# Kernel optimization log

Measured on AMD Instinct MI355X. Metric: run time of the kernel, lower is better.

Reference implementation:

```python
import jax, jax.numpy as jnp
import numpy as np

K_CHUNK = 512  # key-chunk size used by the module when n > 5000


def setup_inputs() -> dict:
    key = jax.random.key(0)
    ks = jax.random.split(key, 9)
    b, n, d = 1, 8192, 512
    s = 1.0 / np.sqrt(d)
    x = jax.random.normal(ks[0], (b, n, d), dtype=jnp.float32)
    Wq = jax.random.normal(ks[1], (d, d), dtype=jnp.float32) * s
    bq = jax.random.normal(ks[2], (d,), dtype=jnp.float32) * 0.01
    Wk = jax.random.normal(ks[3], (d, d), dtype=jnp.float32) * s
    bk = jax.random.normal(ks[4], (d,), dtype=jnp.float32) * 0.01
    Wv = jax.random.normal(ks[5], (d, d), dtype=jnp.float32) * s
    bv = jax.random.normal(ks[6], (d,), dtype=jnp.float32) * 0.01
    Wo = jax.random.normal(ks[7], (d, d), dtype=jnp.float32) * s
    bo = jax.random.normal(ks[8], (d,), dtype=jnp.float32) * 0.01
    return {"x": x, "Wq": Wq, "bq": bq, "Wk": Wk, "bk": bk,
            "Wv": Wv, "bv": bv, "Wo": Wo, "bo": bo}


def reference(x, Wq, bq, Wk, bk, Wv, bv, Wo, bo):
    # Faithful to the n > 5000 branch of SimpleAttenLayer (eval mode: dropout = identity).
    # The q-chunking in the original does not change the math (each q row is independent),
    # so we vectorize over all queries. The k-chunking DOES change the math: softmax is
    # applied within each 512-wide key block, then a second softmax over the concatenated
    # per-block weights, then matmul with full v.
    b, n, d = x.shape
    assert n % K_CHUNK == 0
    q = x @ Wq + bq
    k = x @ Wk + bk
    v = x @ Wv + bv
    scores = jnp.einsum('bnd,bmd->bnm', q, k) / jnp.sqrt(jnp.float32(d))
    # softmax within each key chunk of size K_CHUNK
    w1 = jax.nn.softmax(scores.reshape(b, n, n // K_CHUNK, K_CHUNK), axis=-1)
    w1 = w1.reshape(b, n, n)
    # second (global) softmax over the concatenated chunk weights
    w2 = jax.nn.softmax(w1, axis=-1)
    attn_out = jnp.einsum('bnm,bmd->bnd', w2, v)
    cls_attn_weights = w2[:, 0:1, :]  # [b, 1, n]
    out = x + (attn_out @ Wo + bo)
    return (out, cls_attn_weights)
```

## Files before the change

### kernel.cpp

```cpp
#include <hip/hip_runtime.h>
#include <stdint.h>

typedef unsigned short u16;
typedef uint8_t u8;
typedef __bf16 bf16x8 __attribute__((ext_vector_type(8)));
typedef float f32x4 __attribute__((ext_vector_type(4)));

#define NTOK 8192
#define DD 512
#define CHK 512
#define NCH 16
#define KSPLIT 4
#define KLEN 2048
#define LOG2E 1.4426950408889634f
#define SCL 0.044194173824159216f
#define SCLL 0.063762069130835270f

__device__ __forceinline__ u16 f2bf(float f) {
  union { float f; uint32_t u; } v; v.f = f;
  uint32_t r = v.u + 0x7FFFu + ((v.u >> 16) & 1u);
  return (u16)(r >> 16);
}

template <int CTRL>
__device__ __forceinline__ float dppadd(float x) {
  int y = __builtin_amdgcn_update_dpp(0, __float_as_int(x), CTRL, 0xF, 0xF, true);
  return x + __int_as_float(y);
}
__device__ __forceinline__ float rowsum16(float x) {
  x = dppadd<0xB1>(x);
  x = dppadd<0x4E>(x);
  x = dppadd<0x141>(x);
  x = dppadd<0x140>(x);
  return x;
}

typedef const __attribute__((address_space(1))) unsigned int* gas_t;
typedef __attribute__((address_space(3))) unsigned int* las_t;
__device__ __forceinline__ void gload16(const void* g, void* l) {
  __builtin_amdgcn_global_load_lds((gas_t)g, (las_t)l, 16, 0, 0);
}

__device__ __forceinline__ int permtok(int t) {
  return (t & ~63) | (((t & 15) << 2) | ((t >> 4) & 3));
}

__global__ void prep_kernel(const float* __restrict__ x, const float* __restrict__ Wq,
                            const float* __restrict__ Wk, const float* __restrict__ Wv,
                            const float* __restrict__ Wo, const float* __restrict__ bq,
                            u16* __restrict__ xb, u16* __restrict__ Wall, u16* __restrict__ WoT,
                            float* __restrict__ lsum, float* __restrict__ q0g) {
  __shared__ float t[32][33];
  const int bid = blockIdx.x;
  const int tid = threadIdx.x;
  if (bid < 4096) {
    int i = bid * 256 + tid;
    if (bid < 32) lsum[bid * 256 + tid] = 0.f;
    float4 v = ((const float4*)x)[i];
    ushort4 o;
    o.x = f2bf(v.x); o.y = f2bf(v.y); o.z = f2bf(v.z); o.w = f2bf(v.w);
    ((ushort4*)xb)[i] = o;
  } else if (bid < 5120) {
    const int tt = bid - 4096;
    const int z = tt >> 8, idx = tt & 255;
    const float* W; u16* WT;
    if (z == 0)      { W = Wq; WT = Wall; }
    else if (z == 1) { W = Wk; WT = Wall + 512 * 512; }
    else if (z == 2) { W = Wv; WT = Wall + 2 * 512 * 512; }
    else             { W = Wo; WT = WoT; }
    const int n0 = (idx & 15) * 32, k0 = (idx >> 4) * 32;
    const int tx = tid & 31, ty = tid >> 5;
    #pragma unroll
    for (int i = 0; i < 4; i++)
      t[ty + 8 * i][tx] = W[(k0 + ty + 8 * i) * DD + n0 + tx];
    __syncthreads();
    #pragma unroll
    for (int i = 0; i < 4; i++)
      WT[(n0 + ty + 8 * i) * DD + k0 + tx] = f2bf(t[tx][ty + 8 * i]);
  } else {
    const int c = (bid - 5120) * 256 + tid;
    float acc = bq[c];
    #pragma unroll 8
    for (int i = 0; i < 512; i++) acc += x[i] * Wq[i * 512 + c];
    q0g[c] = acc;
  }
}

__launch_bounds__(256, 3)
__global__ void qkv_kernel(const u16* __restrict__ A, const u16* __restrict__ Wall,
                           const float* __restrict__ bq, const float* __restrict__ bk,
                           const float* __restrict__ bv, u8* __restrict__ qb8,
                           u8* __restrict__ kb8, u8* __restrict__ vT8) {
  __shared__ __align__(16) u16 As[128 * 32];
  __shared__ __align__(16) u16 Bs[128 * 32];
  const int m0 = blockIdx.x * 128;
  const int n0g = blockIdx.y * 128;
  const int which = blockIdx.y >> 2;
  const int n0 = n0g & 511;
  const int tid = threadIdx.x;
  const int w = tid >> 6, lane = tid & 63, lm = lane & 15, quad = lane >> 4;
  const int wm = w & 1, wn = w >> 1;
  f32x4 acc[4][4] = {};
  const int soff = tid * 16;
  const int srow = soff >> 6;
  const int scol = soff & 63;
  const char* Ag = (const char*)A + ((size_t)(m0 + srow) * DD) * 2 + scol;
  const char* Bg = (const char*)Wall + ((size_t)(n0g + srow) * DD) * 2 + scol;
  char* Al = (char*)As + w * 1024;
  char* Bl = (char*)Bs + w * 1024;
  const size_t rs = (size_t)64 * DD * 2;
  for (int kk = 0; kk < DD; kk += 32) {
    const char* ag = Ag + (size_t)kk * 2;
    const char* bg = Bg + (size_t)kk * 2;
    gload16(ag, Al);
    gload16(ag + rs, Al + 4096);
    gload16(bg, Bl);
    gload16(bg + rs, Bl + 4096);
    __syncthreads();
    bf16x8 af[4], bfr[4];
    #pragma unroll
    for (int i = 0; i < 4; i++) af[i] = *(const bf16x8*)&As[(wm * 64 + i * 16 + lm) * 32 + quad * 8];
    #pragma unroll
    for (int j = 0; j < 4; j++) bfr[j] = *(const bf16x8*)&Bs[(wn * 64 + j * 16 + lm) * 32 + quad * 8];
    #pragma unroll
    for (int i = 0; i < 4; i++)
      #pragma unroll
      for (int j = 0; j < 4; j++)
        acc[i][j] = __builtin_amdgcn_mfma_f32_16x16x32_bf16(af[i], bfr[j], acc[i][j], 0, 0, 0);
    __syncthreads();
  }
  const float* bias = (which == 0) ? bq : (which == 1) ? bk : bv;
  #pragma unroll
  for (int i = 0; i < 4; i++) {
    const int row0 = m0 + wm * 64 + i * 16 + quad * 4;
    #pragma unroll
    for (int j = 0; j < 4; j++) {
      const int col = n0 + wn * 64 + j * 16 + lm;
      const float bv_ = bias[col];
      if (which == 2) {
        #pragma unroll
        for (int r = 0; r < 4; r++) {
          const float val = acc[i][j][r] + bv_;
          uint32_t pk = __builtin_amdgcn_cvt_pk_fp8_f32(val, val, 0, false);
          vT8[(size_t)col * NTOK + permtok(row0 + r)] = (u8)(pk & 0xFF);
        }
      } else {
        u8* dst = (which == 0) ? qb8 : kb8;
        #pragma unroll
        for (int r = 0; r < 4; r++) {
          const float val = acc[i][j][r] + bv_;
          uint32_t pk = __builtin_amdgcn_cvt_pk_fp8_f32(val, val, 0, false);
          dst[(size_t)(row0 + r) * DD + col] = (u8)(pk & 0xFF);
        }
      }
    }
  }
}

__launch_bounds__(256, 3)
__global__ void outproj_kernel(const u16* __restrict__ A, const u16* __restrict__ BT,
                               const float* __restrict__ bias, float* __restrict__ outp,
                               const float* __restrict__ resid) {
  __shared__ __align__(16) u16 As[128 * 32];
  __shared__ __align__(16) u16 Bs[128 * 32];
  const int m0 = blockIdx.x * 128, n0 = blockIdx.y * 128;
  const int tid = threadIdx.x;
  const int w = tid >> 6, lane = tid & 63, lm = lane & 15, quad = lane >> 4;
  const int wm = w & 1, wn = w >> 1;
  f32x4 acc[4][4] = {};
  const int soff = tid * 16;
  const int srow = soff >> 6;
  const int scol = soff & 63;
  const char* Ag = (const char*)A + ((size_t)(m0 + srow) * DD) * 2 + scol;
  const char* Bg = (const char*)BT + ((size_t)(n0 + srow) * DD) * 2 + scol;
  char* Al = (char*)As + w * 1024;
  char* Bl = (char*)Bs + w * 1024;
  const size_t rs = (size_t)64 * DD * 2;
  for (int kk = 0; kk < DD; kk += 32) {
    const char* ag = Ag + (size_t)kk * 2;
    const char* bg = Bg + (size_t)kk * 2;
    gload16(ag, Al);
    gload16(ag + rs, Al + 4096);
    gload16(bg, Bl);
    gload16(bg + rs, Bl + 4096);
    __syncthreads();
    bf16x8 af[4], bfr[4];
    #pragma unroll
    for (int i = 0; i < 4; i++) af[i] = *(const bf16x8*)&As[(wm * 64 + i * 16 + lm) * 32 + quad * 8];
    #pragma unroll
    for (int j = 0; j < 4; j++) bfr[j] = *(const bf16x8*)&Bs[(wn * 64 + j * 16 + lm) * 32 + quad * 8];
    #pragma unroll
    for (int i = 0; i < 4; i++)
      #pragma unroll
      for (int j = 0; j < 4; j++)
        acc[i][j] = __builtin_amdgcn_mfma_f32_16x16x32_bf16(af[i], bfr[j], acc[i][j], 0, 0, 0);
    __syncthreads();
  }
  #pragma unroll
  for (int i = 0; i < 4; i++) {
    const int row0 = m0 + wm * 64 + i * 16 + quad * 4;
    #pragma unroll
    for (int j = 0; j < 4; j++) {
      const int col = n0 + wn * 64 + j * 16 + lm;
      const float bv = bias[col];
      #pragma unroll
      for (int r = 0; r < 4; r++) {
        const size_t idx = (size_t)(row0 + r) * DD + col;
        outp[idx] = acc[i][j][r] + bv + resid[idx];
      }
    }
  }
}

template <int MODE>
__launch_bounds__(256, 3)
__global__ void gemm_fp8_kernel(const u8* __restrict__ A, const u8* __restrict__ BT,
                                int K, int lda, int ldb, void* __restrict__ outp,
                                const float* __restrict__ lsum) {
  __shared__ __align__(16) u8 As[128 * 64];
  __shared__ __align__(16) u8 Bs[128 * 64];
  const int m0 = blockIdx.x * 128, n0 = blockIdx.y * 128;
  const int tid = threadIdx.x;
  const int w = tid >> 6, lane = tid & 63, lm = lane & 15, quad = lane >> 4;
  const int wm = w & 1, wn = w >> 1;
  f32x4 acc[4][4] = {};
  const int srow = tid >> 2;
  const int scol = ((tid & 3) ^ ((srow >> 1) & 3)) * 16;
  const size_t kbase = (MODE == 4) ? (size_t)blockIdx.z * (size_t)K : 0;
  const u8* Ag = A + (size_t)(m0 + srow) * lda + kbase + scol;
  const u8* Bg = BT + (size_t)(n0 + srow) * ldb + kbase + scol;
  u8* Al = As + w * 1024;
  u8* Bl = Bs + w * 1024;
  const size_t ars = (size_t)64 * lda;
  const size_t brs = (size_t)64 * ldb;
  const int swz = (lm >> 1) & 3;
  const int off8 = (quad & 1) * 8;
  const int cg0 = quad >> 1;
  for (int kk = 0; kk < K; kk += 64) {
    const u8* ag = Ag + kk;
    const u8* bg = Bg + kk;
    gload16(ag, Al);
    gload16(ag + ars, Al + 4096);
    gload16(bg, Bl);
    gload16(bg + brs, Bl + 4096);
    __syncthreads();
    #pragma unroll
    for (int kk2 = 0; kk2 < 64; kk2 += 32) {
      const int csel = ((cg0 + (kk2 >> 4)) ^ swz) * 16 + off8;
      long af[4], bfr[4];
      #pragma unroll
      for (int i = 0; i < 4; i++)
        af[i] = *(const long*)&As[(wm * 64 + i * 16 + lm) * 64 + csel];
      #pragma unroll
      for (int j = 0; j < 4; j++)
        bfr[j] = *(const long*)&Bs[(wn * 64 + j * 16 + lm) * 64 + csel];
      #pragma unroll
      for (int i = 0; i < 4; i++)
        #pragma unroll
        for (int j = 0; j < 4; j++)
          acc[i][j] = __builtin_amdgcn_mfma_f32_16x16x32_fp8_fp8(af[i], bfr[j], acc[i][j], 0, 0, 0);
    }
    __syncthreads();
  }
  #pragma unroll
  for (int i = 0; i < 4; i++) {
    const int row0 = m0 + wm * 64 + i * 16 + quad * 4;
    float li[4];
    if (MODE == 3) {
      #pragma unroll
      for (int r = 0; r < 4; r++) li[r] = 1.0f / lsum[row0 + r];
    }
    #pragma unroll
    for (int j = 0; j < 4; j++) {
      const int col = n0 + wn * 64 + j * 16 + lm;
      if (MODE == 3) {
        #pragma unroll
        for (int r = 0; r < 4; r++)
          ((u16*)outp)[(size_t)(row0 + r) * DD + col] = f2bf(acc[i][j][r] * li[r]);
      } else {
        float* po = (float*)outp + (size_t)blockIdx.z * NTOK * DD;
        #pragma unroll
        for (int r = 0; r < 4; r++)
          po[(size_t)(row0 + r) * DD + col] = acc[i][j][r];
      }
    }
  }
}

__global__ void pv_reduce_kernel(const float* __restrict__ part, const float* __restrict__ lsum,
                                 u16* __restrict__ attnb) {
  const int idx = blockIdx.x * 256 + threadIdx.x;
  const int row = idx >> 7;
  const int c4 = (idx & 127) << 2;
  const float* p = part + (size_t)row * DD + c4;
  const size_t stride = (size_t)NTOK * DD;
  float4 a = *(const float4*)(p);
  float4 b = *(const float4*)(p + stride);
  float4 c = *(const float4*)(p + 2 * stride);
  float4 d = *(const float4*)(p + 3 * stride);
  const float inv = 1.0f / lsum[row];
  ushort4 o;
  o.x = f2bf((a.x + b.x + c.x + d.x) * inv);
  o.y = f2bf((a.y + b.y + c.y + d.y) * inv);
  o.z = f2bf((a.z + b.z + c.z + d.z) * inv);
  o.w = f2bf((a.w + b.w + c.w + d.w) * inv);
  *(ushort4*)(attnb + (size_t)row * DD + c4) = o;
}

__launch_bounds__(1024, 4)
__global__ void scores_kernel(const u8* __restrict__ qb8, const u8* __restrict__ kb8,
                              u8* __restrict__ P8, float* __restrict__ lsum) {
  __shared__ __align__(16) u8 As[128 * 64];
  __shared__ __align__(16) u8 Bs[512 * 64];
  __shared__ float hS[8][128], hP[8][128], hZ[128];
  const int m0 = blockIdx.x * 128;
  const int c = blockIdx.y;
  const int tid = threadIdx.x;
  const int w = tid >> 6, lane = tid & 63, lm = lane & 15, quad = lane >> 4;
  const int mt = w & 1, wsl = w >> 1;
  f32x4 s[4][4] = {};
  const int srA = tid >> 2;
  const int scS = ((tid & 3) ^ ((srA >> 1) & 3)) * 16;
  const u8* Qg = qb8 + (size_t)(m0 + srA) * DD + scS;
  const u8* Kg = kb8 + (size_t)(c * CHK + srA) * DD + scS;
  u8* Al = As + w * 1024;
  u8* Bl = Bs + w * 1024;
  const int swz = (lm >> 1) & 3;
  const int off8 = (quad & 1) * 8;
  const int cg0 = quad >> 1;
  for (int kk = 0; kk < DD; kk += 64) {
    if (tid < 512) gload16(Qg + kk, Al);
    gload16(Kg + kk, Bl);
    gload16(Kg + kk + (size_t)256 * DD, Bl + 16384);
    __syncthreads();
    #pragma unroll
    for (int kk2 = 0; kk2 < 64; kk2 += 32) {
      const int csel = ((cg0 + (kk2 >> 4)) ^ swz) * 16 + off8;
      long af[4], bfr[4];
      #pragma unroll
      for (int i = 0; i < 4; i++)
        af[i] = *(const long*)&As[(mt * 64 + i * 16 + lm) * 64 + csel];
      #pragma unroll
      for (int j = 0; j < 4; j++)
        bfr[j] = *(const long*)&Bs[(wsl * 64 + j * 16 + lm) * 64 + csel];
      #pragma unroll
      for (int i = 0; i < 4; i++)
        #pragma unroll
        for (int j = 0; j < 4; j++)
          s[i][j] = __builtin_amdgcn_mfma_f32_16x16x32_fp8_fp8(af[i], bfr[j], s[i][j], 0, 0, 0);
    }
    __syncthreads();
  }
  #pragma unroll
  for (int i = 0; i < 4; i++) {
    #pragma unroll
    for (int reg = 0; reg < 4; reg++) {
      float z = 0.f;
      #pragma unroll
      for (int j = 0; j < 4; j++) {
        float e = exp2f(s[i][j][reg] * SCLL);
        s[i][j][reg] = e;
        z += e;
      }
      z = rowsum16(z);
      if (lm == 0) hS[wsl][mt * 64 + i * 16 + quad * 4 + reg] = z;
    }
  }
  __syncthreads();
  if (tid < 128) {
    float t = 0.f;
    #pragma unroll
    for (int w2 = 0; w2 < 8; w2++) t += hS[w2][tid];
    hZ[tid] = LOG2E / t;
  }
  __syncthreads();
  #pragma unroll
  for (int i = 0; i < 4; i++) {
    #pragma unroll
    for (int reg = 0; reg < 4; reg++) {
      const int rl = mt * 64 + i * 16 + quad * 4 + reg;
      const float iz = hZ[rl];
      const float p0 = exp2f(s[i][0][reg] * iz);
      const float p1 = exp2f(s[i][1][reg] * iz);
      const float p2 = exp2f(s[i][2][reg] * iz);
      const float p3 = exp2f(s[i][3][reg] * iz);
      float zp = (p0 + p1) + (p2 + p3);
      zp = rowsum16(zp);
      if (lm == 0) hP[wsl][rl] = zp;
      uint32_t o = __builtin_amdgcn_cvt_pk_fp8_f32(p0, p1, 0, false);
      o = __builtin_amdgcn_cvt_pk_fp8_f32(p2, p3, o, true);
      *(uint32_t*)(P8 + (size_t)(m0 + rl) * NTOK + c * CHK + wsl * 64 + lm * 4) = o;
    }
  }
  __syncthreads();
  if (tid < 128) {
    float t = 0.f;
    #pragma unroll
    for (int w2 = 0; w2 < 8; w2++) t += hP[w2][tid];
    atomicAdd(&lsum[m0 + tid], t);
  }
}

__global__ void cls_u_kernel(const float* __restrict__ Wk, const float* __restrict__ bk,
                             const float* __restrict__ q0g, float* __restrict__ uc) {
  __shared__ float q0[512];
  const int tid = threadIdx.x;
  q0[tid] = q0g[tid];
  q0[tid + 256] = q0g[tid + 256];
  __syncthreads();
  if (blockIdx.x < 8) {
    const int c = blockIdx.x * 64 + (tid >> 2), ii = tid & 3;
    float acc = 0.f;
    #pragma unroll 8
    for (int j = ii; j < 512; j += 4) acc += Wk[(size_t)c * 512 + j] * q0[j];
    acc += __shfl_xor(acc, 1, 64);
    acc += __shfl_xor(acc, 2, 64);
    if (ii == 0) uc[c] = acc;
  } else if (tid < 64) {
    float acc = 0.f;
    #pragma unroll 8
    for (int j = tid; j < 512; j += 64) acc += bk[j] * q0[j];
    #pragma unroll
    for (int off = 1; off < 64; off <<= 1) acc += __shfl_xor(acc, off, 64);
    if (tid == 0) uc[512] = acc;
  }
}

__global__ void cls_scores_kernel(const float* __restrict__ x, const float* __restrict__ uc,
                                  float* __restrict__ s0) {
  __shared__ float u[512];
  __shared__ float c0s;
  int tid = threadIdx.x;
  for (int i = tid; i < 512; i += 256) u[i] = uc[i];
  if (tid == 0) c0s = uc[512];
  __syncthreads();
  int rowg = blockIdx.x * 32 + (tid >> 3);
  int ii = tid & 7;
  const float* xr = x + rowg * 512;
  float acc = 0.f;
  for (int i = ii; i < 512; i += 8) acc += xr[i] * u[i];
  acc += __shfl_xor(acc, 1, 64);
  acc += __shfl_xor(acc, 2, 64);
  acc += __shfl_xor(acc, 4, 64);
  if (ii == 0) s0[rowg] = (acc + c0s) * SCL;
}

__global__ void cls_softmax_kernel(const float* __restrict__ s0, float* __restrict__ out) {
  int tid = threadIdx.x;
  int w = tid >> 6, lane = tid & 63;
  const float* sc = s0 + w * 512;
  float v[8];
  float m = -1e30f;
  #pragma unroll
  for (int j = 0; j < 8; j++) { v[j] = sc[lane * 8 + j]; m = fmaxf(m, v[j]); }
  for (int off = 1; off < 64; off <<= 1) m = fmaxf(m, __shfl_xor(m, off, 64));
  float z = 0.f;
  #pragma unroll
  for (int j = 0; j < 8; j++) { v[j] = expf(v[j] - m); z += v[j]; }
  for (int off = 1; off < 64; off <<= 1) z += __shfl_xor(z, off, 64);
  float invz = 1.f / z;
  float l = 0.f;
  #pragma unroll
  for (int j = 0; j < 8; j++) { v[j] = expf(v[j] * invz); l += v[j]; }
  for (int off = 1; off < 64; off <<= 1) l += __shfl_xor(l, off, 64);
  __shared__ float lw[16];
  if (lane == 0) lw[w] = l;
  __syncthreads();
  float L = 0.f;
  for (int i = 0; i < 16; i++) L += lw[i];
  float invL = 1.f / L;
  #pragma unroll
  for (int j = 0; j < 8; j++) out[w * 512 + lane * 8 + j] = v[j] * invL;
}

extern "C" void kernel_launch(void* const* d_in, const int* in_sizes, int n_in,
                              void* d_out, int out_size, void* d_ws, size_t ws_size,
                              hipStream_t stream) {
  const float* x  = (const float*)d_in[0];
  const float* Wq = (const float*)d_in[1];
  const float* bq = (const float*)d_in[2];
  const float* Wk = (const float*)d_in[3];
  const float* bk = (const float*)d_in[4];
  const float* Wv = (const float*)d_in[5];
  const float* bv = (const float*)d_in[6];
  const float* Wo = (const float*)d_in[7];
  const float* bo = (const float*)d_in[8];
  float* out = (float*)d_out;

  char* ws = (char*)d_ws;
  u16* xb    = (u16*)(ws);
  u16* Wall  = (u16*)(ws + 8388608);
  u16* WoT   = (u16*)(ws + 9961472);
  u8*  qb8   = (u8*)(ws + 10485760);
  u8*  kb8   = (u8*)(ws + 14680064);
  u8*  vT8   = (u8*)(ws + 18874368);
  u16* attnb = (u16*)(ws + 23068672);
  float* q0g = (float*)(ws + 31457280);
  float* uc  = (float*)(ws + 31461376);
  float* s0  = (float*)(ws + 31465472);
  float* lsum= (float*)(ws + 31498240);
  u8*  P8    = (u8*)(ws + 31531008);
  float* part= (float*)(ws + 98639872);
  const size_t need_full = 98639872ULL + (size_t)KSPLIT * NTOK * DD * 4ULL;

  prep_kernel<<<5122, 256, 0, stream>>>(x, Wq, Wk, Wv, Wo, bq, xb, Wall, WoT, lsum, q0g);

  qkv_kernel<<<dim3(NTOK / 128, 12), 256, 0, stream>>>(xb, Wall, bq, bk, bv, qb8, kb8, vT8);

  scores_kernel<<<dim3(NTOK / 128, NCH), 1024, 0, stream>>>(qb8, kb8, P8, lsum);

  if (ws_size >= need_full) {
    gemm_fp8_kernel<4><<<dim3(NTOK / 128, DD / 128, KSPLIT), 256, 0, stream>>>(
        P8, vT8, KLEN, NTOK, NTOK, part, nullptr);
    pv_reduce_kernel<<<NTOK * DD / 4 / 256, 256, 0, stream>>>(part, lsum, attnb);
  } else {
    gemm_fp8_kernel<3><<<dim3(NTOK / 128, DD / 128), 256, 0, stream>>>(
        P8, vT8, NTOK, NTOK, NTOK, attnb, lsum);
  }

  outproj_kernel<<<dim3(NTOK / 128, DD / 128), 256, 0, stream>>>(attnb, WoT, bo, out, x);

  cls_u_kernel<<<9, 256, 0, stream>>>(Wk, bk, q0g, uc);
  cls_scores_kernel<<<NTOK / 32, 256, 0, stream>>>(x, uc, s0);
  cls_softmax_kernel<<<1, 1024, 0, stream>>>(s0, out + (size_t)NTOK * DD);
}
```

Measured before the change: 330.7 us.

## Interleave fp8 K-dimension layout so each lane loads 16 bytes per MFMA pair

Result: faster. 314.9 us (-4.8%).

```diff
diff --git a/kernel.cpp b/kernel.cpp
--- a/kernel.cpp
+++ b/kernel.cpp
@@ -5,6 +5,7 @@
 typedef uint8_t u8;
 typedef __bf16 bf16x8 __attribute__((ext_vector_type(8)));
 typedef float f32x4 __attribute__((ext_vector_type(4)));
+typedef long i64x2 __attribute__((ext_vector_type(2)));
 
 #define NTOK 8192
 #define DD 512
@@ -41,8 +42,13 @@
   __builtin_amdgcn_global_load_lds((gas_t)g, (las_t)l, 16, 0, 0);
 }
 
-__device__ __forceinline__ int permtok(int t) {
-  return (t & ~63) | (((t & 15) << 2) | ((t >> 4) & 3));
+__device__ __forceinline__ int ilv64(int p) {
+  const int g = p >> 3;
+  return (((g & 3) * 2) + (g >> 2)) * 8 + (p & 7);
+}
+__device__ __forceinline__ int fperm(int t) {
+  const int p = ((t & 15) << 2) | ((t >> 4) & 3);
+  return (t & ~63) | ilv64(p);
 }
 
 __global__ void prep_kernel(const float* __restrict__ x, const float* __restrict__ Wq,
@@ -142,15 +148,16 @@
         for (int r = 0; r < 4; r++) {
           const float val = acc[i][j][r] + bv_;
           uint32_t pk = __builtin_amdgcn_cvt_pk_fp8_f32(val, val, 0, false);
-          vT8[(size_t)col * NTOK + permtok(row0 + r)] = (u8)(pk & 0xFF);
+          vT8[(size_t)col * NTOK + fperm(row0 + r)] = (u8)(pk & 0xFF);
         }
       } else {
         u8* dst = (which == 0) ? qb8 : kb8;
+        const int icol = (col & ~63) | ilv64(col & 63);
         #pragma unroll
         for (int r = 0; r < 4; r++) {
           const float val = acc[i][j][r] + bv_;
           uint32_t pk = __builtin_amdgcn_cvt_pk_fp8_f32(val, val, 0, false);
-          dst[(size_t)(row0 + r) * DD + col] = (u8)(pk & 0xFF);
+          dst[(size_t)(row0 + r) * DD + icol] = (u8)(pk & 0xFF);
         }
       }
     }
@@ -233,9 +240,7 @@
   u8* Bl = Bs + w * 1024;
   const size_t ars = (size_t)64 * lda;
   const size_t brs = (size_t)64 * ldb;
-  const int swz = (lm >> 1) & 3;
-  const int off8 = (quad & 1) * 8;
-  const int cg0 = quad >> 1;
+  const int csel = ((quad ^ ((lm >> 1) & 3)) * 16);
   for (int kk = 0; kk < K; kk += 64) {
     const u8* ag = Ag + kk;
     const u8* bg = Bg + kk;
@@ -244,22 +249,20 @@
     gload16(bg, Bl);
     gload16(bg + brs, Bl + 4096);
     __syncthreads();
-    #pragma unroll
-    for (int kk2 = 0; kk2 < 64; kk2 += 32) {
-      const int csel = ((cg0 + (kk2 >> 4)) ^ swz) * 16 + off8;
-      long af[4], bfr[4];
-      #pragma unroll
-      for (int i = 0; i < 4; i++)
-        af[i] = *(const long*)&As[(wm * 64 + i * 16 + lm) * 64 + csel];
-      #pragma unroll
-      for (int j = 0; j < 4; j++)
-        bfr[j] = *(const long*)&Bs[(wn * 64 + j * 16 + lm) * 64 + csel];
-      #pragma unroll
-      for (int i = 0; i < 4; i++)
-        #pragma unroll
-        for (int j = 0; j < 4; j++)
-          acc[i][j] = __builtin_amdgcn_mfma_f32_16x16x32_fp8_fp8(af[i], bfr[j], acc[i][j], 0, 0, 0);
-    }
+    i64x2 afv[4], bfv[4];
+    #pragma unroll
+    for (int i = 0; i < 4; i++)
+      afv[i] = *(const i64x2*)&As[(wm * 64 + i * 16 + lm) * 64 + csel];
+    #pragma unroll
+    for (int j = 0; j < 4; j++)
+      bfv[j] = *(const i64x2*)&Bs[(wn * 64 + j * 16 + lm) * 64 + csel];
+    #pragma unroll
+    for (int i = 0; i < 4; i++)
+      #pragma unroll
+      for (int j = 0; j < 4; j++) {
+        acc[i][j] = __builtin_amdgcn_mfma_f32_16x16x32_fp8_fp8(afv[i].x, bfv[j].x, acc[i][j], 0, 0, 0);
+        acc[i][j] = __builtin_amdgcn_mfma_f32_16x16x32_fp8_fp8(afv[i].y, bfv[j].y, acc[i][j], 0, 0, 0);
+      }
     __syncthreads();
   }
   #pragma unroll
@@ -325,30 +328,26 @@
   const u8* Kg = kb8 + (size_t)(c * CHK + srA) * DD + scS;
   u8* Al = As + w * 1024;
   u8* Bl = Bs + w * 1024;
-  const int swz = (lm >> 1) & 3;
-  const int off8 = (quad & 1) * 8;
-  const int cg0 = quad >> 1;
+  const int csel = ((quad ^ ((lm >> 1) & 3)) * 16);
   for (int kk = 0; kk < DD; kk += 64) {
     if (tid < 512) gload16(Qg + kk, Al);
     gload16(Kg + kk, Bl);
     gload16(Kg + kk + (size_t)256 * DD, Bl + 16384);
     __syncthreads();
-    #pragma unroll
-    for (int kk2 = 0; kk2 < 64; kk2 += 32) {
-      const int csel = ((cg0 + (kk2 >> 4)) ^ swz) * 16 + off8;
-      long af[4], bfr[4];
-      #pragma unroll
-      for (int i = 0; i < 4; i++)
-        af[i] = *(const long*)&As[(mt * 64 + i * 16 + lm) * 64 + csel];
-      #pragma unroll
-      for (int j = 0; j < 4; j++)
-        bfr[j] = *(const long*)&Bs[(wsl * 64 + j * 16 + lm) * 64 + csel];
-      #pragma unroll
-      for (int i = 0; i < 4; i++)
-        #pragma unroll
-        for (int j = 0; j < 4; j++)
-          s[i][j] = __builtin_amdgcn_mfma_f32_16x16x32_fp8_fp8(af[i], bfr[j], s[i][j], 0, 0, 0);
-    }
+    i64x2 afv[4], bfv[4];
+    #pragma unroll
+    for (int i = 0; i < 4; i++)
+      afv[i] = *(const i64x2*)&As[(mt * 64 + i * 16 + lm) * 64 + csel];
+    #pragma unroll
+    for (int j = 0; j < 4; j++)
+      bfv[j] = *(const i64x2*)&Bs[(wsl * 64 + j * 16 + lm) * 64 + csel];
+    #pragma unroll
+    for (int i = 0; i < 4; i++)
+      #pragma unroll
+      for (int j = 0; j < 4; j++) {
+        s[i][j] = __builtin_amdgcn_mfma_f32_16x16x32_fp8_fp8(afv[i].x, bfv[j].x, s[i][j], 0, 0, 0);
+        s[i][j] = __builtin_amdgcn_mfma_f32_16x16x32_fp8_fp8(afv[i].y, bfv[j].y, s[i][j], 0, 0, 0);
+      }
     __syncthreads();
   }
   #pragma unroll
@@ -374,6 +373,8 @@
     hZ[tid] = LOG2E / t;
   }
   __syncthreads();
+  const int newc = ((lm >> 1) & 3) * 2 + (lm >> 3);
+  const int pbyte = wsl * 64 + newc * 8 + (lm & 1) * 4;
   #pragma unroll
   for (int i = 0; i < 4; i++) {
     #pragma unroll
@@ -389,7 +390,7 @@
       if (lm == 0) hP[wsl][rl] = zp;
       uint32_t o = __builtin_amdgcn_cvt_pk_fp8_f32(p0, p1, 0, false);
       o = __builtin_amdgcn_cvt_pk_fp8_f32(p2, p3, o, true);
-      *(uint32_t*)(P8 + (size_t)(m0 + rl) * NTOK + c * CHK + wsl * 64 + lm * 4) = o;
+      *(uint32_t*)(P8 + (size_t)(m0 + rl) * NTOK + c * CHK + pbyte) = o;
     }
   }
   __syncthreads();
```
